# Kernel optimization log

Measured on AMD Instinct MI355X. Metric: run time of the kernel, lower is better.

The kernel has to match this reference:

```python
import jax, jax.numpy as jnp
import numpy as np

TEMPERATURE = 0.5
EPS = 1e-10

N, C, H, W = 8, 256, 96, 96
T, V = 32, 256
NUM_CLASSES = 19


def setup_inputs() -> dict:
    key = jax.random.key(0)
    k1, k2, k3, k4 = jax.random.split(key, 4)
    features = jax.random.normal(k1, (N, C, H, W), dtype=jnp.float32)
    batch_inds = jax.random.randint(k2, (T,), 0, N, dtype=jnp.int32)
    sample_inds = jax.random.randint(k3, (T, V), 0, H * W).astype(jnp.int64)
    labels = jax.random.randint(k4, (T,), 0, NUM_CLASSES, dtype=jnp.int32)
    return {"features": features, "batch_inds": batch_inds,
            "sample_inds": sample_inds, "labels": labels}


def reference(features, batch_inds, sample_inds, labels):
    n, c, h, w = features.shape
    t, v = sample_inds.shape
    # --- anchor sampling: gather V pixels per (image, class) pair ---
    f = features.reshape(n, c, h * w)            # (N, C, HW)
    g = f[batch_inds]                            # (T, C, HW)
    sampled = jnp.take_along_axis(g, sample_inds[:, None, :], axis=2)  # (T, C, V)
    # --- contrastive loss ---
    norm = jnp.maximum(jnp.linalg.norm(sampled, axis=1, keepdims=True), 1e-12)
    feats = sampled / norm                       # L2 normalize along C
    feats = jnp.swapaxes(feats, 1, 2).reshape(t * v, c)  # (T*V, C)
    lab = jnp.repeat(labels, v)                  # (T*V,)
    dot = (feats @ feats.T) / TEMPERATURE        # (T*V, T*V)
    eq = (lab[:, None] == lab[None, :]).astype(dot.dtype)
    diag = jnp.eye(t * v, dtype=dot.dtype)
    pos_mask = eq * (1.0 - diag)
    neg_mask = 1.0 - eq
    # stable SupCon loss: logsumexp over {self-exp + all negatives}
    logits = dot - jax.lax.stop_gradient(jnp.max(dot, axis=1, keepdims=True))
    exp_logits = jnp.exp(logits)
    neg_sum = jnp.sum(exp_logits * neg_mask, axis=1, keepdims=True)
    log_prob = logits - jnp.log(exp_logits + neg_sum)
    mean_log_prob_pos = jnp.sum(pos_mask * log_prob, axis=1) / jnp.maximum(
        jnp.sum(pos_mask, axis=1), EPS)
    return -jnp.mean(mean_log_prob_pos)
```

## Files before the change

kernel.cpp:

```cpp
#include <hip/hip_runtime.h>
#include <hip/hip_bf16.h>


namespace {

constexpr int kC = 256;
constexpr int kHW = 96 * 96;
constexpr int kT = 32;
constexpr int kV = 256;
constexpr int kM = kT * kV;

typedef __attribute__((ext_vector_type(8))) short short8;
typedef __attribute__((ext_vector_type(4))) float f32x4;

__device__ inline unsigned short f2bf(float x) {
  __hip_bfloat16 h = __float2bfloat16(x);
  return __builtin_bit_cast(unsigned short, h);
}
__device__ inline float bf2f(unsigned short u) {
  unsigned int v = ((unsigned int)u) << 16;
  return __builtin_bit_cast(float, v);
}
__device__ inline void load_lds16(const unsigned short* g, unsigned short* l) {
  __builtin_amdgcn_global_load_lds(
      (const __attribute__((address_space(1))) void*)g,
      (__attribute__((address_space(3))) void*)l, 16, 0, 0);
}

__device__ inline void stage_tile4(const unsigned short* __restrict__ F,
                                   unsigned short* lds, int ct, int tid) {
#pragma unroll
  for (int i = 0; i < 8; ++i) {
    const int n = i * 256 + tid;
    const int j = n >> 5;
    const int m = (n & 31) ^ (j & 31);
    load_lds16(F + ((size_t)(ct * 64 + j) << 8) + m * 8,
               lds + (size_t)n * 8);
  }
}

__device__ inline void stage_tile8(const unsigned short* __restrict__ F,
                                   unsigned short* lds, int ct, int tid) {
#pragma unroll
  for (int i = 0; i < 4; ++i) {
    const int n = i * 512 + tid;
    const int j = n >> 5;
    const int m = (n & 31) ^ (j & 31);
    load_lds16(F + ((size_t)(ct * 64 + j) << 8) + m * 8,
               lds + (size_t)n * 8);
  }
}

}

__global__ __launch_bounds__(256) void k_prep(
    const int* __restrict__ labels, float* __restrict__ ns,
    float* __restrict__ out, int out_size, int* __restrict__ nact,
    ushort2* __restrict__ list, float* __restrict__ cscale) {
  const int tid = (int)threadIdx.x;
  const int b = (int)blockIdx.x;
  for (int i = b * 256 + tid; i < kM; i += 64 * 256) ns[i] = 0.f;
  if (b != 0) return;
  __shared__ int s_lab[kT];
  if (tid < kT) s_lab[tid] = labels[tid];
  if (tid == 0) *nact = 0;
  for (int i = tid; i < out_size; i += 256) out[i] = 0.f;
  __syncthreads();
  if (tid < kT) {
    int m = 0;
    for (int u = 0; u < kT; ++u) m += (s_lab[u] == s_lab[tid]) ? 1 : 0;
    cscale[tid] = 1.f / ((float)(m * kV - 1) * (float)kM);
  }
  for (int p = tid; p < kT * kT; p += 256) {
    const int ti = p >> 5, tj = p & 31;
    if (s_lab[ti] == s_lab[tj]) {
      int base = atomicAdd(nact, 16);
#pragma unroll
      for (int a = 0; a < 4; ++a)
#pragma unroll
        for (int bb = 0; bb < 4; ++bb) {
          ushort2 e;
          e.x = (unsigned short)(ti * 4 + a);
          e.y = (unsigned short)(tj * 4 + bb);
          list[base + a * 4 + bb] = e;
        }
    }
  }
}

__global__ __launch_bounds__(256) void k_gather(
    const float* __restrict__ feat, const int* __restrict__ binds,
    const int* __restrict__ sinds, unsigned short* __restrict__ FT) {
  const int b = (int)blockIdx.x;
  const int c = (int)blockIdx.y;
  __shared__ alignas(16) float row[kHW];
  __shared__ int s_match[kT + 1];
  if (threadIdx.x == 0) {
    int cnt = 0;
    for (int t = 0; t < kT; ++t)
      if (binds[t] == b) s_match[1 + cnt++] = t;
    s_match[0] = cnt;
  }
  __syncthreads();
  const int cnt = s_match[0];
  if (cnt == 0) return;
  const float4* src4 = (const float4*)(feat + ((size_t)b * kC + c) * kHW);
  for (int i = (int)threadIdx.x; i < kHW / 4; i += 256)
    ((float4*)row)[i] = src4[i];
  __syncthreads();
  unsigned short* dst = FT + (size_t)c * kM;
  for (int mi = 1; mi <= cnt; ++mi) {
    const int t = s_match[mi];
    const int p = sinds[t * kV + threadIdx.x];
    dst[t * kV + threadIdx.x] = f2bf(row[p]);
  }
}

__global__ __launch_bounds__(256) void k_norm(
    const unsigned short* __restrict__ FT, unsigned short* __restrict__ F) {
  constexpr int PAD = 40;
  const int v0 = (int)blockIdx.x * 32;
  __shared__ alignas(16) unsigned short tile[kC][PAD];
  __shared__ float part[8][32];
  __shared__ float s_inv[32];
  const int tid = (int)threadIdx.x;
  {
    const int p4 = tid & 3, cb = tid >> 2;
    for (int c = cb; c < kC; c += 64) {
      int4 d = *(const int4*)(FT + (size_t)c * kM + v0 + p4 * 8);
      *(int4*)&tile[c][p4 * 8] = d;
    }
  }
  __syncthreads();
  {
    const int v = tid & 31, oct = tid >> 5;
    float ss = 0.f;
    for (int c = oct * 32; c < oct * 32 + 32; ++c) {
      float x = bf2f(tile[c][v]);
      ss += x * x;
    }
    part[oct][v] = ss;
  }
  __syncthreads();
  if (tid < 32) {
    float ss = 0.f;
#pragma unroll
    for (int o = 0; o < 8; ++o) ss += part[o][tid];
    s_inv[tid] = 1.0f / fmaxf(sqrtf(ss), 1e-12f);
  }
  __syncthreads();
#pragma unroll
  for (int p = 0; p < 4; ++p) {
    const int chunk = p * 256 + tid;
    const int v = chunk >> 5, c0 = (chunk & 31) << 3;
    const float inv = s_inv[v];
    alignas(16) unsigned short o[8];
#pragma unroll
    for (int k = 0; k < 8; ++k) o[k] = f2bf(bf2f(tile[c0 + k][v]) * inv);
    *(int4*)(F + (size_t)(v0 + v) * kC + c0) = *(const int4*)o;
  }
}

__global__ __launch_bounds__(512, 4) void k_neg(
    const unsigned short* __restrict__ F, const int* __restrict__ labels,
    float* __restrict__ ns) {
  const int tid = (int)threadIdx.x;
  const int w = tid >> 6, lane = tid & 63, q = lane >> 4, l16 = lane & 15;
  const int wr = w >> 1, wc = w & 1;
  const int bid = (int)blockIdx.x;
  const int panel = bid & 7;
  const int rb = bid >> 3;
  const int row0 = rb * 128;
  __shared__ alignas(16) unsigned short Bt[64 * kC];
  __shared__ int s_lab[kT];
  __shared__ int s_tiles[16];
  __shared__ int s_nt;
  __shared__ float s_red[8][32];
  if (tid < kT) s_lab[tid] = labels[tid];
  __syncthreads();
  const int labr = s_lab[rb >> 1];
  if (tid == 0) {
    int n = 0;
    for (int ct = panel * 16; ct < panel * 16 + 16; ++ct)
      if (s_lab[ct >> 2] != labr) s_tiles[n++] = ct;
    s_nt = n;
  }
  __syncthreads();
  const int nt = s_nt;
  if (nt == 0) return;

  short8 af[2][8];
  stage_tile8(F, Bt, rb * 2, tid);
  __syncthreads();
  if (wr < 2) {
#pragma unroll
    for (int rg = 0; rg < 2; ++rg) {
      const int ja = wr * 32 + rg * 16 + l16;
      const unsigned short* arow = Bt + ja * kC;
#pragma unroll
      for (int ks = 0; ks < 8; ++ks)
        af[rg][ks] =
            *(const short8*)(arow + (((ks * 4 + q) ^ (ja & 31)) << 3));
    }
  }
  __syncthreads();
  stage_tile8(F, Bt, rb * 2 + 1, tid);
  __syncthreads();
  if (wr >= 2) {
#pragma unroll
    for (int rg = 0; rg < 2; ++rg) {
      const int ja = (wr - 2) * 32 + rg * 16 + l16;
      const unsigned short* arow = Bt + ja * kC;
#pragma unroll
      for (int ks = 0; ks < 8; ++ks)
        af[rg][ks] =
            *(const short8*)(arow + (((ks * 4 + q) ^ (ja & 31)) << 3));
    }
  }

  const unsigned short* bc0 = Bt + (wc * 32 + l16) * kC;
  const unsigned short* bc1 = bc0 + 16 * kC;
  int bofs[8];
#pragma unroll
  for (int ks = 0; ks < 8; ++ks) bofs[ks] = ((ks * 4 + q) ^ l16) << 3;

  float sacc[2][4] = {};
  for (int it = 0; it < nt; ++it) {
    __syncthreads();
    stage_tile8(F, Bt, s_tiles[it], tid);
    __syncthreads();
    f32x4 a00 = {0.f, 0.f, 0.f, 0.f}, a01 = a00, a10 = a00, a11 = a00;
#pragma unroll
    for (int ks = 0; ks < 8; ++ks) {
      short8 b0 = *(const short8*)(bc0 + bofs[ks]);
      short8 b1 = *(const short8*)(bc1 + (bofs[ks] ^ 128));
      a00 = __builtin_amdgcn_mfma_f32_16x16x32_bf16(af[0][ks], b0, a00, 0, 0, 0);
      a01 = __builtin_amdgcn_mfma_f32_16x16x32_bf16(af[0][ks], b1, a01, 0, 0, 0);
      a10 = __builtin_amdgcn_mfma_f32_16x16x32_bf16(af[1][ks], b0, a10, 0, 0, 0);
      a11 = __builtin_amdgcn_mfma_f32_16x16x32_bf16(af[1][ks], b1, a11, 0, 0, 0);
    }
#pragma unroll
    for (int r = 0; r < 4; ++r) {
      sacc[0][r] += __expf(fmaf(a00[r], 2.f, -2.f)) +
                    __expf(fmaf(a01[r], 2.f, -2.f));
      sacc[1][r] += __expf(fmaf(a10[r], 2.f, -2.f)) +
                    __expf(fmaf(a11[r], 2.f, -2.f));
    }
  }

#pragma unroll
  for (int rg = 0; rg < 2; ++rg)
#pragma unroll
    for (int r = 0; r < 4; ++r) {
      float v = sacc[rg][r];
      v += __shfl_xor(v, 1, 64);
      v += __shfl_xor(v, 2, 64);
      v += __shfl_xor(v, 4, 64);
      v += __shfl_xor(v, 8, 64);
      if (l16 == 0) s_red[w][rg * 16 + q * 4 + r] = v;
    }
  __syncthreads();
  if (tid < 128) {
    const int rr = tid >> 5, e = tid & 31;
    float v = s_red[rr * 2][e] + s_red[rr * 2 + 1][e];
    atomicAdd(&ns[row0 + tid], v);
  }
}

__global__ __launch_bounds__(256, 3) void k_pos(
    const unsigned short* __restrict__ F, const float* __restrict__ ns,
    const int* __restrict__ nact, const ushort2* __restrict__ list,
    const float* __restrict__ cscale, float* __restrict__ out) {
  const int tid = (int)threadIdx.x;
  const int w = tid >> 6, lane = tid & 63, q = lane >> 4, l16 = lane & 15;
  const int wr = w >> 1, wc = w & 1;
  __shared__ alignas(16) unsigned short Bt[64 * kC];
  __shared__ float s_pos[4];
  const int n = *nact;

  const int jb0 = wc * 32 + l16, jb1 = wc * 32 + 16 + l16;
  int bofs0[8], bofs1[8];
#pragma unroll
  for (int ks = 0; ks < 8; ++ks) {
    bofs0[ks] = (((ks * 4 + q) ^ (jb0 & 31)) << 3);
    bofs1[ks] = (((ks * 4 + q) ^ (jb1 & 31)) << 3);
  }
  const unsigned short* bc0 = (const unsigned short*)Bt + jb0 * kC;
  const unsigned short* bc1 = (const unsigned short*)Bt + jb1 * kC;

  float pos = 0.f;
  for (int idx = (int)blockIdx.x; idx < n; idx += (int)gridDim.x) {
    const ushort2 e = list[idx];
    const int bi = e.x, bj = e.y;
    stage_tile4(F, Bt, bj, tid);

    short8 af[2][8];
#pragma unroll
    for (int rg = 0; rg < 2; ++rg) {
      const int row = bi * 64 + wr * 32 + rg * 16 + l16;
#pragma unroll
      for (int ks = 0; ks < 8; ++ks)
        af[rg][ks] = *(const short8*)((const short*)F + (size_t)row * kC +
                                      ks * 32 + q * 8);
    }
    float nsv[2][4];
#pragma unroll
    for (int rg = 0; rg < 2; ++rg)
#pragma unroll
      for (int r = 0; r < 4; ++r)
        nsv[rg][r] = ns[bi * 64 + wr * 32 + rg * 16 + q * 4 + r];
    const float scale = cscale[bi >> 2];

    __syncthreads();

    f32x4 a00 = {0.f, 0.f, 0.f, 0.f}, a01 = a00, a10 = a00, a11 = a00;
#pragma unroll
    for (int ks = 0; ks < 8; ++ks) {
      short8 b0 = *(const short8*)(bc0 + bofs0[ks]);
      short8 b1 = *(const short8*)(bc1 + bofs1[ks]);
      a00 = __builtin_amdgcn_mfma_f32_16x16x32_bf16(af[0][ks], b0, a00, 0, 0, 0);
      a01 = __builtin_amdgcn_mfma_f32_16x16x32_bf16(af[0][ks], b1, a01, 0, 0, 0);
      a10 = __builtin_amdgcn_mfma_f32_16x16x32_bf16(af[1][ks], b0, a10, 0, 0, 0);
      a11 = __builtin_amdgcn_mfma_f32_16x16x32_bf16(af[1][ks], b1, a11, 0, 0, 0);
    }

    float tpos = 0.f;
#pragma unroll
    for (int rg = 0; rg < 2; ++rg)
#pragma unroll
      for (int cg = 0; cg < 2; ++cg) {
        const f32x4 acc = (rg == 0) ? (cg == 0 ? a00 : a01)
                                    : (cg == 0 ? a10 : a11);
        const int jc = bj * 64 + wc * 32 + cg * 16 + l16;
#pragma unroll
        for (int r = 0; r < 4; ++r) {
          const int i = bi * 64 + wr * 32 + rg * 16 + q * 4 + r;
          if (i != jc) {
            float d = fmaf(acc[r], 2.f, -2.f);
            tpos += d - __logf(__expf(d) + nsv[rg][r]);
          }
        }
      }
    pos += scale * tpos;
    __syncthreads();
  }

#pragma unroll
  for (int m = 1; m < 64; m <<= 1) pos += __shfl_xor(pos, m, 64);
  if (lane == 0) s_pos[w] = pos;
  __syncthreads();
  if (tid == 0)
    atomicAdd(out, -(s_pos[0] + s_pos[1] + s_pos[2] + s_pos[3]));
}

extern "C" void kernel_launch(void* const* d_in, const int* in_sizes, int n_in,
                              void* d_out, int out_size, void* d_ws,
                              size_t ws_size, hipStream_t stream) {
  const float* feat = (const float*)d_in[0];
  const int* binds = (const int*)d_in[1];
  const int* sinds = (const int*)d_in[2];
  const int* labels = (const int*)d_in[3];
  float* out = (float*)d_out;
  unsigned short* FT = (unsigned short*)d_ws;
  unsigned short* F = FT + (size_t)kC * kM;
  float* ns = (float*)(F + (size_t)kM * kC);
  int* nact = (int*)(ns + kM);
  float* cscale = (float*)(nact + 8);
  ushort2* list = (ushort2*)(cscale + 32);

  k_prep<<<64, 256, 0, stream>>>(labels, ns, out, out_size, nact, list, cscale);
  k_gather<<<dim3(8, kC), 256, 0, stream>>>(feat, binds, sinds, FT);
  k_norm<<<kM / 32, 256, 0, stream>>>(FT, F);
  k_neg<<<dim3(512), 512, 0, stream>>>(F, labels, ns);
  k_pos<<<768, 256, 0, stream>>>(F, ns, nact, list, cscale, out);
}
```

Before: 178.5 us.

## Double-buffer LDS tiles in negative-sum kernel and fold exp scaling into exp2

The negative-sum kernel now keeps two LDS tile buffers. It prefetches the next column tile while MFMAs run on the current one, which leaves one barrier per iteration instead of two. The two A-row tiles are staged at once instead of one after the other, and the exponent's scale is folded into a single exp2 FMA. The cost is that LDS per block doubles to about 64KB, which can cut the number of resident blocks per CU below the launch-bounds target of 4.

```diff
diff --git a/kernel.cpp b/kernel.cpp
--- a/kernel.cpp
+++ b/kernel.cpp
@@ -25,6 +25,10 @@
   __builtin_amdgcn_global_load_lds(
       (const __attribute__((address_space(1))) void*)g,
       (__attribute__((address_space(3))) void*)l, 16, 0, 0);
+}
+
+__device__ inline float exp_2am2(float a) {
+  return exp2f(fmaf(a, 2.8853900818f, -2.8853900818f));
 }
 
 __device__ inline void stage_tile4(const unsigned short* __restrict__ F,
@@ -171,7 +175,7 @@
   const int panel = bid & 7;
   const int rb = bid >> 3;
   const int row0 = rb * 128;
-  __shared__ alignas(16) unsigned short Bt[64 * kC];
+  __shared__ alignas(16) unsigned short Bt[2][64 * kC];
   __shared__ int s_lab[kT];
   __shared__ int s_tiles[16];
   __shared__ int s_nt;
@@ -189,14 +193,17 @@
   const int nt = s_nt;
   if (nt == 0) return;
 
+  stage_tile8(F, Bt[0], rb * 2, tid);
+  stage_tile8(F, Bt[1], rb * 2 + 1, tid);
+  __syncthreads();
   short8 af[2][8];
-  stage_tile8(F, Bt, rb * 2, tid);
-  __syncthreads();
-  if (wr < 2) {
+  {
+    const unsigned short* abuf = Bt[wr >> 1];
+    const int wl = wr & 1;
 #pragma unroll
     for (int rg = 0; rg < 2; ++rg) {
-      const int ja = wr * 32 + rg * 16 + l16;
-      const unsigned short* arow = Bt + ja * kC;
+      const int ja = wl * 32 + rg * 16 + l16;
+      const unsigned short* arow = abuf + ja * kC;
 #pragma unroll
       for (int ks = 0; ks < 8; ++ks)
         af[rg][ks] =
@@ -204,31 +211,20 @@
     }
   }
   __syncthreads();
-  stage_tile8(F, Bt, rb * 2 + 1, tid);
-  __syncthreads();
-  if (wr >= 2) {
-#pragma unroll
-    for (int rg = 0; rg < 2; ++rg) {
-      const int ja = (wr - 2) * 32 + rg * 16 + l16;
-      const unsigned short* arow = Bt + ja * kC;
-#pragma unroll
-      for (int ks = 0; ks < 8; ++ks)
-        af[rg][ks] =
-            *(const short8*)(arow + (((ks * 4 + q) ^ (ja & 31)) << 3));
-    }
-  }
-
-  const unsigned short* bc0 = Bt + (wc * 32 + l16) * kC;
-  const unsigned short* bc1 = bc0 + 16 * kC;
+
+  const int jrow = wc * 32 + l16;
   int bofs[8];
 #pragma unroll
   for (int ks = 0; ks < 8; ++ks) bofs[ks] = ((ks * 4 + q) ^ l16) << 3;
+
+  stage_tile8(F, Bt[0], s_tiles[0], tid);
 
   float sacc[2][4] = {};
   for (int it = 0; it < nt; ++it) {
     __syncthreads();
-    stage_tile8(F, Bt, s_tiles[it], tid);
-    __syncthreads();
+    if (it + 1 < nt) stage_tile8(F, Bt[(it + 1) & 1], s_tiles[it + 1], tid);
+    const unsigned short* bc0 = Bt[it & 1] + jrow * kC;
+    const unsigned short* bc1 = bc0 + 16 * kC;
     f32x4 a00 = {0.f, 0.f, 0.f, 0.f}, a01 = a00, a10 = a00, a11 = a00;
 #pragma unroll
     for (int ks = 0; ks < 8; ++ks) {
@@ -241,10 +237,8 @@
     }
 #pragma unroll
     for (int r = 0; r < 4; ++r) {
-      sacc[0][r] += __expf(fmaf(a00[r], 2.f, -2.f)) +
-                    __expf(fmaf(a01[r], 2.f, -2.f));
-      sacc[1][r] += __expf(fmaf(a10[r], 2.f, -2.f)) +
-                    __expf(fmaf(a11[r], 2.f, -2.f));
+      sacc[0][r] += exp_2am2(a00[r]) + exp_2am2(a01[r]);
+      sacc[1][r] += exp_2am2(a10[r]) + exp_2am2(a11[r]);
     }
   }
 
```

Result: slower. 187.7 us (+5.1%).
